# Kernel tuning notes

Hardware: AMD Instinct MI355X
Metric: run time of the kernel (lower is better)

The kernel has to match this reference:

```python
import jax, jax.numpy as jnp
import numpy as np

B, N, Kn, D, L = 4, 2048, 30, 128, 3

def setup_inputs():
    key = jax.random.key(0)
    ks = jax.random.split(key, 16)
    def nrm(k, shape, fan_in):
        return jax.random.normal(k, shape, dtype=jnp.float32) * (1.0 / np.sqrt(fan_in))
    return {
        "V": jax.random.normal(ks[0], (B, N, D), dtype=jnp.float32),
        "E": jax.random.normal(ks[1], (B, N, Kn, D), dtype=jnp.float32),
        "K": jax.random.randint(ks[2], (B, N, Kn), 0, N),
        "Z": jax.random.normal(ks[3], (B, N, D), dtype=jnp.float32),
        "t": jax.random.uniform(ks[4], (B,), dtype=jnp.float32) * 999.0 + 1.0,
        "edge_mask": jnp.ones((B, N, Kn), dtype=bool),
        "sm_W1": nrm(ks[5], (2 * D, D), 2 * D),
        "sm_b1": jnp.zeros((D,), jnp.float32),
        "sm_W2": nrm(ks[6], (D, D), D),
        "sm_b2": jnp.zeros((D,), jnp.float32),
        "sm_ada_W": nrm(ks[7], (D, 2 * D), D),
        "sm_ada_b": jnp.zeros((2 * D,), jnp.float32),
        "msg_W1": nrm(ks[8], (L, 3 * D, D), 3 * D),
        "msg_b1": jnp.zeros((L, D), jnp.float32),
        "msg_W2": nrm(ks[9], (L, D, D), D),
        "msg_b2": jnp.zeros((L, D), jnp.float32),
        "ada1_W": nrm(ks[10], (L, D, 2 * D), D),
        "ada1_b": jnp.zeros((L, 2 * D), jnp.float32),
        "ffn_W1": nrm(ks[11], (L, D, D), D),
        "ffn_b1": jnp.zeros((L, D), jnp.float32),
        "ffn_W2": nrm(ks[12], (L, D, D), D),
        "ffn_b2": jnp.zeros((L, D), jnp.float32),
        "ada2_W": nrm(ks[13], (L, D, 2 * D), D),
        "ada2_b": jnp.zeros((L, 2 * D), jnp.float32),
        "proj_W": nrm(ks[14], (D, D), D),
    }

def _ln(x):
    mu = x.mean(-1, keepdims=True)
    var = ((x - mu) ** 2).mean(-1, keepdims=True)
    return (x - mu) * jax.lax.rsqrt(var + 1e-5)

def _adaln(x, tf, W, b):
    # adaLN: LayerNorm (no affine) modulated by time features -> scale/shift
    g, bt = jnp.split(tf @ W + b, 2, axis=-1)  # each [B,1,D]
    return _ln(x) * (1.0 + g) + bt

def _featurize_t(t):
    wn = 10000.0 ** (-jnp.arange(0, D, 2, dtype=jnp.float32) / D)   # [D/2]
    phase = t[:, None, None] * wn[None, None, :]                    # [B,1,D/2]
    tf = jnp.stack([jnp.sin(phase), jnp.cos(phase)], axis=-1)       # [B,1,D/2,2] interleaved sin/cos
    return tf.reshape(t.shape[0], 1, D)

def reference(V, E, K, Z, t, edge_mask, sm_W1, sm_b1, sm_W2, sm_b2, sm_ada_W, sm_ada_b,
              msg_W1, msg_b1, msg_W2, msg_b2, ada1_W, ada1_b, ffn_W1, ffn_b1,
              ffn_W2, ffn_b2, ada2_W, ada2_b, proj_W):
    tf = _featurize_t(t)                                 # [B,1,D]
    VZ = jnp.concatenate([V, Z], axis=-1)                # [B,N,2D]
    h = jax.nn.gelu(VZ @ sm_W1 + sm_b1) @ sm_W2 + sm_b2  # sequence messenger MLP
    V = _adaln(V + h, tf, sm_ada_W, sm_ada_b)
    bidx = jnp.arange(V.shape[0])[:, None, None]
    for l in range(L):
        Vj = V[bidx, K]                                  # gather neighbors [B,N,Kn,D]
        Vi = jnp.broadcast_to(V[:, :, None, :], Vj.shape)
        Min = jnp.concatenate([Vi, E, Vj], axis=-1)      # [B,N,Kn,3D]
        msg = jax.nn.gelu(Min @ msg_W1[l] + msg_b1[l]) @ msg_W2[l] + msg_b2[l]
        msg = jnp.where(edge_mask[..., None], msg, 0.0)
        dV = msg.sum(axis=2) / Kn                        # aggregate over neighbors
        V = _adaln(V + dV, tf, ada1_W[l], ada1_b[l])
        h = jax.nn.gelu(V @ ffn_W1[l] + ffn_b1[l]) @ ffn_W2[l] + ffn_b2[l]
        V = _adaln(V + h, tf, ada2_W[l], ada2_b[l])
    return V @ proj_W
```

## Files before the change

kernel.cpp:

```cpp
#include <hip/hip_runtime.h>
#include <hip/hip_bf16.h>

#define DEV static __device__ __forceinline__

typedef __bf16 bf16x8 __attribute__((ext_vector_type(8)));
typedef unsigned short u16x8 __attribute__((ext_vector_type(8)));
typedef unsigned short u16x4 __attribute__((ext_vector_type(4)));
typedef float f32x4 __attribute__((ext_vector_type(4)));

#if __has_builtin(__builtin_amdgcn_exp2f)
#define EXP2F(x) __builtin_amdgcn_exp2f(x)
#else
#define EXP2F(x) exp2f(x)
#endif
#if __has_builtin(__builtin_amdgcn_rcpf)
#define RCPF(x) __builtin_amdgcn_rcpf(x)
#else
#define RCPF(x) (1.0f / (x))
#endif


DEV unsigned short f2bfh(float f) {
    return __builtin_bit_cast(unsigned short, (__bf16)f);
}

DEV float bf2f(unsigned short v) {
    return __builtin_bit_cast(float, (unsigned)v << 16);
}

DEV float gelu_f(float x) {
    float x2 = x * x;
    float t  = __builtin_fmaf(-0.10294324f, x2, -2.3022082f);
    float e  = EXP2F(x * t);
    return x * RCPF(1.0f + e);
}

DEV f32x4 mfma16(bf16x8 a, bf16x8 b, f32x4 c) {
    return __builtin_amdgcn_mfma_f32_16x16x32_bf16(a, b, c, 0, 0, 0);
}

DEV bf16x8 cvt8(float4 x, float4 y) {
    bf16x8 r;
    r[0] = (__bf16)x.x; r[1] = (__bf16)x.y; r[2] = (__bf16)x.z; r[3] = (__bf16)x.w;
    r[4] = (__bf16)y.x; r[5] = (__bf16)y.y; r[6] = (__bf16)y.z; r[7] = (__bf16)y.w;
    return r;
}

DEV bf16x8 aload_f32(const float* p) {
    float4 x = *(const float4*)p;
    float4 y = *(const float4*)(p + 4);
    return cvt8(x, y);
}

DEV bf16x8 uload(const unsigned short* p) {
    return __builtin_bit_cast(bf16x8, *(const u16x8*)(p));
}

DEV bf16x8 bload(const unsigned short* WT, int col, int koff) {
    return __builtin_bit_cast(bf16x8, *(const u16x8*)(WT + col * 136 + koff));
}

DEV void stage_wt(unsigned short* WT, const unsigned short* src, int tid, int nthr) {
    for (int i = tid; i < 2048; i += nthr) {
        int n = i >> 4, k0 = (i & 15) << 3;
        *(u16x8*)(WT + n * 136 + k0) = *(const u16x8*)(src + n * 128 + k0);
    }
}

__global__ __launch_bounds__(256) void k_wconv(
    const float* __restrict__ smW1, const float* __restrict__ smW2,
    const float* __restrict__ projW, const float* __restrict__ msgW1,
    const float* __restrict__ msgW2, const float* __restrict__ ffnW1,
    const float* __restrict__ ffnW2, unsigned short* __restrict__ WTG)
{
    int m = blockIdx.x >> 3;
    int chunk = blockIdx.x & 7;
    const float* src;
    if (m == 0) src = smW1;
    else if (m == 1) src = smW1 + 16384;
    else if (m == 2) src = smW2;
    else if (m == 3) src = projW;
    else {
        int mm = m - 4; int l = mm / 6; int j = mm % 6;
        if (j < 3)      src = msgW1 + l * 49152 + j * 16384;
        else if (j == 3) src = msgW2 + l * 16384;
        else if (j == 4) src = ffnW1 + l * 16384;
        else             src = ffnW2 + l * 16384;
    }
    unsigned short* dst = WTG + m * 16384;
    int s0 = chunk * 2048 + threadIdx.x * 8;
    int k = s0 >> 7, n = s0 & 127;
    float4 x = *(const float4*)(src + s0);
    float4 y = *(const float4*)(src + s0 + 4);
    dst[(n + 0) * 128 + k] = f2bfh(x.x);
    dst[(n + 1) * 128 + k] = f2bfh(x.y);
    dst[(n + 2) * 128 + k] = f2bfh(x.z);
    dst[(n + 3) * 128 + k] = f2bfh(x.w);
    dst[(n + 4) * 128 + k] = f2bfh(y.x);
    dst[(n + 5) * 128 + k] = f2bfh(y.y);
    dst[(n + 6) * 128 + k] = f2bfh(y.z);
    dst[(n + 7) * 128 + k] = f2bfh(y.w);
}

__global__ __launch_bounds__(256) void k_prep(
    const float* __restrict__ t,
    const float* __restrict__ smadaW, const float* __restrict__ smadab,
    const float* __restrict__ a1W, const float* __restrict__ a1b,
    const float* __restrict__ a2W, const float* __restrict__ a2b,
    float* __restrict__ MOD)
{
    __shared__ float tf[4][128];
    int tid = threadIdx.x;
    {
        int b = tid >> 6, i = tid & 63;
        float wn = __expf(-(float)i * (9.210340371976184f / 64.0f));
        float ph = t[b] * wn;
        tf[b][2 * i]     = sinf(ph);
        tf[b][2 * i + 1] = cosf(ph);
    }
    __syncthreads();
    int o = blockIdx.x * 256 + tid;
    int b, c;
    const float* W; const float* bias; float* out;
    if (o < 1024) {
        b = o >> 8; c = o & 255; W = smadaW; bias = smadab; out = MOD + o;
    } else if (o < 4096) {
        int oo = o - 1024; int lb = oo >> 8; int l = lb >> 2;
        b = lb & 3; c = oo & 255;
        W = a1W + l * 32768; bias = a1b + l * 256; out = MOD + o;
    } else {
        int oo = o - 4096; int lb = oo >> 8; int l = lb >> 2;
        b = lb & 3; c = oo & 255;
        W = a2W + l * 32768; bias = a2b + l * 256; out = MOD + 4096 + oo;
    }
    float s = bias[c];
    const float* tfb = tf[b];
    #pragma unroll 8
    for (int k = 0; k < 128; ++k) s += tfb[k] * W[k * 256 + c];
    *out = s;
}

__global__ __launch_bounds__(256) void k_msgr(
    const float* __restrict__ V, const float* __restrict__ Z,
    const unsigned short* __restrict__ WTG,
    const float* __restrict__ smb1, const float* __restrict__ smb2,
    const float* __restrict__ MOD, float* __restrict__ Vout)
{
    __shared__ __align__(16) unsigned short WT[128 * 136];
    __shared__ __align__(16) float XB[64 * 132];
    const int tid = threadIdx.x;
    const int w = tid >> 6, l = tid & 63, lr = l & 15, lg = l >> 4;
    const int tok0 = blockIdx.x * 64;
    const int batch = tok0 >> 11;
    const int rowA = tok0 + w * 16 + lr;

    f32x4 acc[8] = {};
    for (int kh = 0; kh < 2; ++kh) {
        __syncthreads();
        stage_wt(WT, WTG + kh * 16384, tid, 256);
        __syncthreads();
        const float* A = (kh == 0) ? V : Z;
        #pragma unroll
        for (int ks = 0; ks < 4; ++ks) {
            bf16x8 a = aload_f32(A + rowA * 128 + ks * 32 + lg * 8);
            #pragma unroll
            for (int c = 0; c < 8; ++c)
                acc[c] = mfma16(a, bload(WT, c * 16 + lr, ks * 32 + lg * 8), acc[c]);
        }
    }
    #pragma unroll
    for (int c = 0; c < 8; ++c) {
        int col = c * 16 + lr;
        float b1v = smb1[col];
        #pragma unroll
        for (int j = 0; j < 4; ++j)
            XB[(w * 16 + lg * 4 + j) * 132 + col] = gelu_f(acc[c][j] + b1v);
    }
    __syncthreads();
    stage_wt(WT, WTG + 2 * 16384, tid, 256);
    __syncthreads();
    f32x4 acc2[8] = {};
    #pragma unroll
    for (int ks = 0; ks < 4; ++ks) {
        bf16x8 a = aload_f32(XB + (w * 16 + lr) * 132 + ks * 32 + lg * 8);
        #pragma unroll
        for (int c = 0; c < 8; ++c)
            acc2[c] = mfma16(a, bload(WT, c * 16 + lr, ks * 32 + lg * 8), acc2[c]);
    }
    const float* MODp = MOD + batch * 256;
    #pragma unroll
    for (int j = 0; j < 4; ++j) {
        int row = tok0 + w * 16 + lg * 4 + j;
        float xv[8], s1 = 0.f, s2 = 0.f;
        #pragma unroll
        for (int c = 0; c < 8; ++c) {
            int col = c * 16 + lr;
            float x = acc2[c][j] + smb2[col] + V[row * 128 + col];
            xv[c] = x; s1 += x; s2 += x * x;
        }
        #pragma unroll
        for (int m = 1; m <= 8; m <<= 1) { s1 += __shfl_xor(s1, m); s2 += __shfl_xor(s2, m); }
        float mu = s1 * (1.0f / 128.0f);
        float var = s2 * (1.0f / 128.0f) - mu * mu;
        float rs = rsqrtf(var + 1e-5f);
        #pragma unroll
        for (int c = 0; c < 8; ++c) {
            int col = c * 16 + lr;
            Vout[row * 128 + col] = (xv[c] - mu) * rs * (1.0f + MODp[col]) + MODp[128 + col];
        }
    }
}

__global__ __launch_bounds__(256) void k_tab(
    const float* __restrict__ Vb, const unsigned short* __restrict__ WTa,
    const unsigned short* __restrict__ WTc, const float* __restrict__ b1,
    float* __restrict__ TAf, unsigned short* __restrict__ TBb)
{
    __shared__ __align__(16) unsigned short WT[128 * 136];
    const int tid = threadIdx.x;
    const int w = tid >> 6, l = tid & 63, lr = l & 15, lg = l >> 4;
    const int tok0 = blockIdx.x * 64;
    const int rowA = tok0 + w * 16 + lr;

    stage_wt(WT, WTa, tid, 256);
    __syncthreads();
    f32x4 acc[8] = {};
    #pragma unroll
    for (int ks = 0; ks < 4; ++ks) {
        bf16x8 a = aload_f32(Vb + rowA * 128 + ks * 32 + lg * 8);
        #pragma unroll
        for (int c = 0; c < 8; ++c)
            acc[c] = mfma16(a, bload(WT, c * 16 + lr, ks * 32 + lg * 8), acc[c]);
    }
    #pragma unroll
    for (int c = 0; c < 8; ++c) {
        int col = c * 16 + lr;
        float b1v = b1[col];
        #pragma unroll
        for (int j = 0; j < 4; ++j) {
            int row = tok0 + w * 16 + lg * 4 + j;
            TAf[row * 128 + col] = acc[c][j] + b1v;
        }
    }
    __syncthreads();
    stage_wt(WT, WTc, tid, 256);
    __syncthreads();
    f32x4 acc2[8] = {};
    #pragma unroll
    for (int ks = 0; ks < 4; ++ks) {
        bf16x8 a = aload_f32(Vb + rowA * 128 + ks * 32 + lg * 8);
        #pragma unroll
        for (int c = 0; c < 8; ++c)
            acc2[c] = mfma16(a, bload(WT, c * 16 + lr, ks * 32 + lg * 8), acc2[c]);
    }
    #pragma unroll
    for (int c = 0; c < 8; ++c) {
        int col = c * 16 + lr;
        #pragma unroll
        for (int j = 0; j < 4; ++j) {
            int row = tok0 + w * 16 + lg * 4 + j;
            TBb[row * 128 + col] = f2bfh(acc2[c][j]);
        }
    }
}

template<int MODE>
__global__ __launch_bounds__(256, 2) void k_edge10(
    const float* __restrict__ E,
    const unsigned short* __restrict__ Ebf,
    unsigned short* __restrict__ EbfW,
    const int* __restrict__ Kidx, const float* __restrict__ TAf,
    const unsigned short* __restrict__ TBb,
    const unsigned short* __restrict__ WTb, float* __restrict__ S)
{
    __shared__ __align__(16) unsigned short ELb[2][32 * 128];
    __shared__ __align__(16) unsigned short TBL[2][32 * 128];
    const int tid = threadIdx.x;
    const int w = tid >> 6, l = tid & 63, lr = l & 15, lg = l >> 4;
    const int nq = w;
    const int t0 = blockIdx.x * 16;
    const int bbase = (t0 >> 11) << 11;

    bf16x8 bfr[8];
    #pragma unroll
    for (int n = 0; n < 2; ++n)
        #pragma unroll
        for (int ks = 0; ks < 4; ++ks)
            bfr[n * 4 + ks] = uload(WTb + (nq * 32 + n * 16 + lr) * 128 + ks * 32 + lg * 8);

    float4 eR[4]; u16x8 eR16[2]; u16x8 tbR[2];
    int ka[2], kb[2], kc[2];

    auto KREAD2 = [&](int tok, int k[2]) {
        #pragma unroll
        for (int it = 0; it < 2; ++it) {
            int r = (it * 256 + tid) >> 4;
            k[it] = (r < 30) ? Kidx[tok * 30 + r] : 0;
        }
    };
    auto EISSUE = [&](int tok) {
        if constexpr (MODE == 2) {
            #pragma unroll
            for (int it = 0; it < 2; ++it)
                eR16[it] = *(const u16x8*)((const char*)Ebf + (size_t)tok * 8192 +
                                           (it * 256 + tid) * 16);
        } else {
            #pragma unroll
            for (int it = 0; it < 4; ++it) {
                int s = it * 256 + tid;
                if (s < 960)
                    eR[it] = *(const float4*)(E + ((size_t)tok * 30 + (s >> 5)) * 128 + (s & 31) * 4);
            }
        }
    };
    auto TBISSUE = [&](const int k[2]) {
        #pragma unroll
        for (int it = 0; it < 2; ++it) {
            int q = (it * 256 + tid) & 15;
            tbR[it] = *(const u16x8*)(TBb + (size_t)(bbase + k[it]) * 128 + q * 8);
        }
    };
    auto SWRITE = [&](int buf, int tok) {
        if constexpr (MODE == 2) {
            #pragma unroll
            for (int it = 0; it < 2; ++it)
                *(u16x8*)((char*)ELb[buf] + (it * 256 + tid) * 16) = eR16[it];
        } else {
            #pragma unroll
            for (int it = 0; it < 4; ++it) {
                int s = it * 256 + tid;
                if (s < 960) {
                    int r = s >> 5, q = s & 31;
                    int soff = r * 256 + ((q * 8) ^ ((r & 7) << 4));
                    u16x4 pk;
                    pk[0] = f2bfh(eR[it].x); pk[1] = f2bfh(eR[it].y);
                    pk[2] = f2bfh(eR[it].z); pk[3] = f2bfh(eR[it].w);
                    *(u16x4*)((char*)ELb[buf] + soff) = pk;
                    if constexpr (MODE == 1)
                        *(u16x4*)((char*)EbfW + (size_t)tok * 8192 + soff) = pk;
                } else if constexpr (MODE == 1) {
                    int r = s >> 5, q = s & 31;
                    int soff = r * 256 + ((q * 8) ^ ((r & 7) << 4));
                    u16x4 z = {0, 0, 0, 0};
                    *(u16x4*)((char*)EbfW + (size_t)tok * 8192 + soff) = z;
                }
            }
        }
        #pragma unroll
        for (int it = 0; it < 2; ++it) {
            int s = it * 256 + tid;
            int r = s >> 4, q = s & 15;
            *(u16x8*)((char*)TBL[buf] + r * 256 + ((q * 16) ^ ((r & 7) << 4))) = tbR[it];
        }
    };

    KREAD2(t0, ka);
    EISSUE(t0);
    TBISSUE(ka);
    KREAD2(t0 + 1, kb);
    SWRITE(0, t0);
    EISSUE(t0 + 1);
    TBISSUE(kb);
    KREAD2(t0 + 2, kc);
    __syncthreads();

    #pragma unroll 1
    for (int i = 0; i < 16; ++i) {
        const int tok = t0 + i;
        const int cur = i & 1;
        float ta[2];
        #pragma unroll
        for (int n = 0; n < 2; ++n) ta[n] = TAf[tok * 128 + nq * 32 + n * 16 + lr];
        float sacc[2] = {0.f, 0.f};
        const char* eb  = (const char*)ELb[cur];
        const char* tbb = (const char*)TBL[cur];
        #pragma unroll
        for (int m = 0; m < 2; ++m) {
            bf16x8 ar[4];
            #pragma unroll
            for (int ks = 0; ks < 4; ++ks)
                ar[ks] = *(const bf16x8*)(eb + (m * 16 + lr) * 256 +
                          (((ks * 32 + lg * 8) * 2) ^ ((lr & 7) << 4)));
            f32x4 acc[2] = {};
            #pragma unroll
            for (int ks = 0; ks < 4; ++ks)
                #pragma unroll
                for (int n = 0; n < 2; ++n)
                    acc[n] = mfma16(ar[ks], bfr[n * 4 + ks], acc[n]);
            #pragma unroll
            for (int n = 0; n < 2; ++n) {
                int c2 = (nq * 32 + n * 16 + lr) * 2;
                #pragma unroll
                for (int j = 0; j < 4; ++j) {
                    int r = m * 16 + lg * 4 + j;
                    if (r < 30) {
                        unsigned short uv = *(const unsigned short*)(tbb + r * 256 + (c2 ^ ((r & 7) << 4)));
                        sacc[n] += gelu_f(acc[n][j] + ta[n] + bf2f(uv));
                    }
                }
            }
        }
        #pragma unroll
        for (int n = 0; n < 2; ++n) {
            sacc[n] += __shfl_xor(sacc[n], 16);
            sacc[n] += __shfl_xor(sacc[n], 32);
        }
        if (l < 16) {
            #pragma unroll
            for (int n = 0; n < 2; ++n)
                S[tok * 128 + nq * 32 + n * 16 + l] = sacc[n];
        }
        if (i < 15) {
            SWRITE(cur ^ 1, t0 + i + 1);
            if (i < 14) {
                EISSUE(t0 + i + 2);
                TBISSUE(kc);
                int tnk = t0 + i + 3; if (tnk > 8191) tnk = 8191;
                KREAD2(tnk, kc);
            }
            __syncthreads();
        }
    }
}

__global__ __launch_bounds__(256) void k_token(
    const float* __restrict__ Sb, const float* __restrict__ Vb,
    const unsigned short* __restrict__ WTW2, const float* __restrict__ b2,
    const unsigned short* __restrict__ WTF1, const float* __restrict__ fb1,
    const unsigned short* __restrict__ WTF2, const float* __restrict__ fb2,
    const unsigned short* __restrict__ WTP,
    const float* __restrict__ MOD1, const float* __restrict__ MOD2,
    float* __restrict__ Vout, int final_)
{
    __shared__ __align__(16) unsigned short WT[128 * 136];
    __shared__ __align__(16) float XB[64 * 132];
    const int tid = threadIdx.x;
    const int w = tid >> 6, l = tid & 63, lr = l & 15, lg = l >> 4;
    const int tok0 = blockIdx.x * 64;
    const int batch = tok0 >> 11;
    const int rloc = w * 16 + lr;

    stage_wt(WT, WTW2, tid, 256);
    __syncthreads();
    f32x4 acc[8] = {};
    #pragma unroll
    for (int ks = 0; ks < 4; ++ks) {
        bf16x8 a = aload_f32(Sb + (tok0 + rloc) * 128 + ks * 32 + lg * 8);
        #pragma unroll
        for (int c = 0; c < 8; ++c)
            acc[c] = mfma16(a, bload(WT, c * 16 + lr, ks * 32 + lg * 8), acc[c]);
    }
    const float* M1 = MOD1 + batch * 256;
    const float* M2 = MOD2 + batch * 256;
    float vp[8][4];
    #pragma unroll
    for (int j = 0; j < 4; ++j) {
        int row = tok0 + w * 16 + lg * 4 + j;
        float xv[8], s1 = 0.f, s2 = 0.f;
        #pragma unroll
        for (int c = 0; c < 8; ++c) {
            int col = c * 16 + lr;
            float x = acc[c][j] * (1.0f / 30.0f) + b2[col] + Vb[row * 128 + col];
            xv[c] = x; s1 += x; s2 += x * x;
        }
        #pragma unroll
        for (int m = 1; m <= 8; m <<= 1) { s1 += __shfl_xor(s1, m); s2 += __shfl_xor(s2, m); }
        float mu = s1 * (1.0f / 128.0f);
        float var = s2 * (1.0f / 128.0f) - mu * mu;
        float rs = rsqrtf(var + 1e-5f);
        #pragma unroll
        for (int c = 0; c < 8; ++c) {
            int col = c * 16 + lr;
            vp[c][j] = (xv[c] - mu) * rs * (1.0f + M1[col]) + M1[128 + col];
        }
    }
    __syncthreads();
    #pragma unroll
    for (int c = 0; c < 8; ++c)
        #pragma unroll
        for (int j = 0; j < 4; ++j)
            XB[(w * 16 + lg * 4 + j) * 132 + c * 16 + lr] = vp[c][j];
    stage_wt(WT, WTF1, tid, 256);
    __syncthreads();
    f32x4 accB[8] = {};
    #pragma unroll
    for (int ks = 0; ks < 4; ++ks) {
        bf16x8 a = aload_f32(XB + rloc * 132 + ks * 32 + lg * 8);
        #pragma unroll
        for (int c = 0; c < 8; ++c)
            accB[c] = mfma16(a, bload(WT, c * 16 + lr, ks * 32 + lg * 8), accB[c]);
    }
    __syncthreads();
    #pragma unroll
    for (int c = 0; c < 8; ++c) {
        int col = c * 16 + lr;
        float bv = fb1[col];
        #pragma unroll
        for (int j = 0; j < 4; ++j)
            XB[(w * 16 + lg * 4 + j) * 132 + col] = gelu_f(accB[c][j] + bv);
    }
    stage_wt(WT, WTF2, tid, 256);
    __syncthreads();
    f32x4 accC[8] = {};
    #pragma unroll
    for (int ks = 0; ks < 4; ++ks) {
        bf16x8 a = aload_f32(XB + rloc * 132 + ks * 32 + lg * 8);
        #pragma unroll
        for (int c = 0; c < 8; ++c)
            accC[c] = mfma16(a, bload(WT, c * 16 + lr, ks * 32 + lg * 8), accC[c]);
    }
    float v2[8][4];
    #pragma unroll
    for (int j = 0; j < 4; ++j) {
        float xv[8], s1 = 0.f, s2 = 0.f;
        #pragma unroll
        for (int c = 0; c < 8; ++c) {
            int col = c * 16 + lr;
            float x = accC[c][j] + fb2[col] + vp[c][j];
            xv[c] = x; s1 += x; s2 += x * x;
        }
        #pragma unroll
        for (int m = 1; m <= 8; m <<= 1) { s1 += __shfl_xor(s1, m); s2 += __shfl_xor(s2, m); }
        float mu = s1 * (1.0f / 128.0f);
        float var = s2 * (1.0f / 128.0f) - mu * mu;
        float rs = rsqrtf(var + 1e-5f);
        #pragma unroll
        for (int c = 0; c < 8; ++c) {
            int col = c * 16 + lr;
            v2[c][j] = (xv[c] - mu) * rs * (1.0f + M2[col]) + M2[128 + col];
        }
    }
    if (!final_) {
        #pragma unroll
        for (int c = 0; c < 8; ++c)
            #pragma unroll
            for (int j = 0; j < 4; ++j)
                Vout[(tok0 + w * 16 + lg * 4 + j) * 128 + c * 16 + lr] = v2[c][j];
    } else {
        __syncthreads();
        #pragma unroll
        for (int c = 0; c < 8; ++c)
            #pragma unroll
            for (int j = 0; j < 4; ++j)
                XB[(w * 16 + lg * 4 + j) * 132 + c * 16 + lr] = v2[c][j];
        stage_wt(WT, WTP, tid, 256);
        __syncthreads();
        f32x4 accD[8] = {};
        #pragma unroll
        for (int ks = 0; ks < 4; ++ks) {
            bf16x8 a = aload_f32(XB + rloc * 132 + ks * 32 + lg * 8);
            #pragma unroll
            for (int c = 0; c < 8; ++c)
                accD[c] = mfma16(a, bload(WT, c * 16 + lr, ks * 32 + lg * 8), accD[c]);
        }
        #pragma unroll
        for (int c = 0; c < 8; ++c)
            #pragma unroll
            for (int j = 0; j < 4; ++j)
                Vout[(tok0 + w * 16 + lg * 4 + j) * 128 + c * 16 + lr] = accD[c][j];
    }
}


extern "C" void kernel_launch(void* const* d_in, const int* in_sizes, int n_in,
                              void* d_out, int out_size, void* d_ws, size_t ws_size,
                              hipStream_t stream)
{
    const float* V     = (const float*)d_in[0];
    const float* E     = (const float*)d_in[1];
    const int*   K     = (const int*)d_in[2];
    const float* Z     = (const float*)d_in[3];
    const float* t     = (const float*)d_in[4];
    const float* smW1   = (const float*)d_in[6];
    const float* smb1   = (const float*)d_in[7];
    const float* smW2   = (const float*)d_in[8];
    const float* smb2   = (const float*)d_in[9];
    const float* smadaW = (const float*)d_in[10];
    const float* smadab = (const float*)d_in[11];
    const float* msgW1  = (const float*)d_in[12];
    const float* msgb1  = (const float*)d_in[13];
    const float* msgW2  = (const float*)d_in[14];
    const float* msgb2  = (const float*)d_in[15];
    const float* a1W    = (const float*)d_in[16];
    const float* a1b    = (const float*)d_in[17];
    const float* fW1    = (const float*)d_in[18];
    const float* fb1    = (const float*)d_in[19];
    const float* fW2    = (const float*)d_in[20];
    const float* fb2    = (const float*)d_in[21];
    const float* a2W    = (const float*)d_in[22];
    const float* a2b    = (const float*)d_in[23];
    const float* projW  = (const float*)d_in[24];

    float* Vbuf = (float*)d_ws;
    float* TAf  = Vbuf + 8192 * 128;
    float* Sb   = TAf + 8192 * 128;
    float* MOD  = Sb + 8192 * 128;
    unsigned short* TBb = (unsigned short*)(MOD + 7168);
    unsigned short* WTG = TBb + 8192 * 128;
    unsigned short* Ebf = WTG + 22 * 16384;

    size_t need = (size_t)(3 * 8192 * 128 + 7168) * 4
                + (size_t)(8192 * 128 + 22 * 16384) * 2
                + (size_t)8192 * 4096 * 2;
    const bool ebf_ok = (ws_size >= need);

    k_wconv<<<dim3(176), dim3(256), 0, stream>>>(smW1, smW2, projW, msgW1, msgW2, fW1, fW2, WTG);
    k_prep<<<dim3(28), dim3(256), 0, stream>>>(t, smadaW, smadab, a1W, a1b, a2W, a2b, MOD);
    k_msgr<<<dim3(128), dim3(256), 0, stream>>>(V, Z, WTG, smb1, smb2, MOD, Vbuf);

    for (int l = 0; l < 3; ++l) {
        const unsigned short* Wl = WTG + (4 + l * 6) * 16384;
        k_tab<<<dim3(128), dim3(256), 0, stream>>>(Vbuf, Wl, Wl + 2 * 16384, msgb1 + l * 128, TAf, TBb);
        if (ebf_ok) {
            if (l == 0)
                k_edge10<1><<<dim3(512), dim3(256), 0, stream>>>(
                    E, Ebf, Ebf, K, TAf, TBb, Wl + 16384, Sb);
            else
                k_edge10<2><<<dim3(512), dim3(256), 0, stream>>>(
                    E, Ebf, Ebf, K, TAf, TBb, Wl + 16384, Sb);
        } else {
            k_edge10<0><<<dim3(512), dim3(256), 0, stream>>>(
                E, Ebf, Ebf, K, TAf, TBb, Wl + 16384, Sb);
        }
        int fin = (l == 2);
        k_token<<<dim3(128), dim3(256), 0, stream>>>(
            Sb, Vbuf, Wl + 3 * 16384, msgb2 + l * 128,
            Wl + 4 * 16384, fb1 + l * 128, Wl + 5 * 16384, fb2 + l * 128,
            WTG + 3 * 16384,
            MOD + 1024 + l * 1024, MOD + 4096 + l * 1024,
            fin ? (float*)d_out : Vbuf, fin);
    }
}
```

Before: 202.4 us.

## Triple-buffer edge kernel and load E/TB tiles directly into LDS

The edge-message kernel moves from double to triple buffering in shared memory and prefetches two tokens ahead. The bf16 E tile and the gathered TB rows are copied with global_load_lds (direct global-to-LDS), which drops the register staging and separate LDS stores; the XOR swizzle is now applied to the global source address. Layer 0 now writes its cached bf16 E copy unswizzled so later layers can swizzle on load. Launch bounds are raised to 3 blocks per SM. The extra buffer increases LDS use, and each load now has to be complete before the barrier, which may limit the occupancy gain.

New measurement: 203.1 us. About the same (+0.3%).

```diff
diff --git a/kernel.cpp b/kernel.cpp
--- a/kernel.cpp
+++ b/kernel.cpp
@@ -65,6 +65,12 @@
         int n = i >> 4, k0 = (i & 15) << 3;
         *(u16x8*)(WT + n * 136 + k0) = *(const u16x8*)(src + n * 128 + k0);
     }
+}
+
+DEV void gload16(const void* g, void* lds) {
+    __builtin_amdgcn_global_load_lds(
+        (const __attribute__((address_space(1))) unsigned*)g,
+        (__attribute__((address_space(3))) unsigned*)lds, 16, 0, 0);
 }
 
 __global__ __launch_bounds__(256) void k_wconv(
@@ -265,7 +271,7 @@
 }
 
 template<int MODE>
-__global__ __launch_bounds__(256, 2) void k_edge10(
+__global__ __launch_bounds__(256, 3) void k_edge11(
     const float* __restrict__ E,
     const unsigned short* __restrict__ Ebf,
     unsigned short* __restrict__ EbfW,
@@ -273,8 +279,8 @@
     const unsigned short* __restrict__ TBb,
     const unsigned short* __restrict__ WTb, float* __restrict__ S)
 {
-    __shared__ __align__(16) unsigned short ELb[2][32 * 128];
-    __shared__ __align__(16) unsigned short TBL[2][32 * 128];
+    __shared__ __align__(16) unsigned short ELb[3][32 * 128];
+    __shared__ __align__(16) unsigned short TBL[3][32 * 128];
     const int tid = threadIdx.x;
     const int w = tid >> 6, l = tid & 63, lr = l & 15, lg = l >> 4;
     const int nq = w;
@@ -288,8 +294,8 @@
         for (int ks = 0; ks < 4; ++ks)
             bfr[n * 4 + ks] = uload(WTb + (nq * 32 + n * 16 + lr) * 128 + ks * 32 + lg * 8);
 
-    float4 eR[4]; u16x8 eR16[2]; u16x8 tbR[2];
-    int ka[2], kb[2], kc[2];
+    float4 eR[4];
+    int kc[2];
 
     auto KREAD2 = [&](int tok, int k[2]) {
         #pragma unroll
@@ -298,76 +304,96 @@
             k[it] = (r < 30) ? Kidx[tok * 30 + r] : 0;
         }
     };
-    auto EISSUE = [&](int tok) {
-        if constexpr (MODE == 2) {
-            #pragma unroll
-            for (int it = 0; it < 2; ++it)
-                eR16[it] = *(const u16x8*)((const char*)Ebf + (size_t)tok * 8192 +
-                                           (it * 256 + tid) * 16);
-        } else {
-            #pragma unroll
-            for (int it = 0; it < 4; ++it) {
-                int s = it * 256 + tid;
-                if (s < 960)
-                    eR[it] = *(const float4*)(E + ((size_t)tok * 30 + (s >> 5)) * 128 + (s & 31) * 4);
-            }
-        }
-    };
-    auto TBISSUE = [&](const int k[2]) {
-        #pragma unroll
-        for (int it = 0; it < 2; ++it) {
-            int q = (it * 256 + tid) & 15;
-            tbR[it] = *(const u16x8*)(TBb + (size_t)(bbase + k[it]) * 128 + q * 8);
-        }
-    };
-    auto SWRITE = [&](int buf, int tok) {
-        if constexpr (MODE == 2) {
-            #pragma unroll
-            for (int it = 0; it < 2; ++it)
-                *(u16x8*)((char*)ELb[buf] + (it * 256 + tid) * 16) = eR16[it];
-        } else {
-            #pragma unroll
-            for (int it = 0; it < 4; ++it) {
-                int s = it * 256 + tid;
-                if (s < 960) {
-                    int r = s >> 5, q = s & 31;
-                    int soff = r * 256 + ((q * 8) ^ ((r & 7) << 4));
-                    u16x4 pk;
-                    pk[0] = f2bfh(eR[it].x); pk[1] = f2bfh(eR[it].y);
-                    pk[2] = f2bfh(eR[it].z); pk[3] = f2bfh(eR[it].w);
-                    *(u16x4*)((char*)ELb[buf] + soff) = pk;
-                    if constexpr (MODE == 1)
-                        *(u16x4*)((char*)EbfW + (size_t)tok * 8192 + soff) = pk;
-                } else if constexpr (MODE == 1) {
-                    int r = s >> 5, q = s & 31;
-                    int soff = r * 256 + ((q * 8) ^ ((r & 7) << 4));
-                    u16x4 z = {0, 0, 0, 0};
-                    *(u16x4*)((char*)EbfW + (size_t)tok * 8192 + soff) = z;
-                }
-            }
-        }
+    auto TBGLOAD = [&](int buf, const int k[2]) {
         #pragma unroll
         for (int it = 0; it < 2; ++it) {
             int s = it * 256 + tid;
             int r = s >> 4, q = s & 15;
-            *(u16x8*)((char*)TBL[buf] + r * 256 + ((q * 16) ^ ((r & 7) << 4))) = tbR[it];
+            const char* src = (const char*)(TBb + (size_t)(bbase + k[it]) * 128)
+                            + (((q ^ (r & 7)) << 4));
+            gload16(src, (char*)TBL[buf] + it * 4096 + (w << 10));
         }
     };
-
-    KREAD2(t0, ka);
-    EISSUE(t0);
-    TBISSUE(ka);
-    KREAD2(t0 + 1, kb);
-    SWRITE(0, t0);
-    EISSUE(t0 + 1);
-    TBISSUE(kb);
-    KREAD2(t0 + 2, kc);
+    auto EGLOAD = [&](int buf, int tok) {
+        #pragma unroll
+        for (int it = 0; it < 2; ++it) {
+            int s = it * 256 + tid;
+            int r = s >> 4, q = s & 15;
+            const char* src = (const char*)Ebf + (size_t)tok * 8192 + r * 256
+                            + (((q ^ (r & 7)) << 4));
+            gload16(src, (char*)ELb[buf] + it * 4096 + (w << 10));
+        }
+    };
+    auto EISSUE = [&](int tok) {
+        #pragma unroll
+        for (int it = 0; it < 4; ++it) {
+            int s = it * 256 + tid;
+            if (s < 960)
+                eR[it] = *(const float4*)(E + ((size_t)tok * 30 + (s >> 5)) * 128 + (s & 31) * 4);
+        }
+    };
+    auto SWRITE_E = [&](int buf, int tok) {
+        #pragma unroll
+        for (int it = 0; it < 4; ++it) {
+            int s = it * 256 + tid;
+            int r = (MODE < 3) ? 0 : 0;
+            if (s < 960) {
+                int rr = s >> 5, q = s & 31;
+                u16x4 pk;
+                pk[0] = f2bfh(eR[it].x); pk[1] = f2bfh(eR[it].y);
+                pk[2] = f2bfh(eR[it].z); pk[3] = f2bfh(eR[it].w);
+                *(u16x4*)((char*)ELb[buf] + rr * 256 + ((q * 8) ^ ((rr & 7) << 4))) = pk;
+                if constexpr (MODE == 1)
+                    *(u16x4*)((char*)EbfW + (size_t)tok * 8192 + rr * 256 + q * 8) = pk;
+            } else if constexpr (MODE == 1) {
+                int rr = s >> 5, q = s & 31;
+                u16x4 z = {0, 0, 0, 0};
+                *(u16x4*)((char*)EbfW + (size_t)tok * 8192 + rr * 256 + q * 8) = z;
+            }
+            (void)r;
+        }
+    };
+
+    if constexpr (MODE == 3) {
+        int ka[2], kb[2];
+        KREAD2(t0, ka);
+        EGLOAD(0, t0);
+        TBGLOAD(0, ka);
+        KREAD2(t0 + 1, kb);
+        EGLOAD(1, t0 + 1);
+        TBGLOAD(1, kb);
+        KREAD2(t0 + 2, kc);
+    } else {
+        int ka[2], kb[2];
+        EISSUE(t0);
+        KREAD2(t0, ka);
+        SWRITE_E(0, t0);
+        TBGLOAD(0, ka);
+        EISSUE(t0 + 1);
+        KREAD2(t0 + 1, kb);
+        SWRITE_E(1, t0 + 1);
+        TBGLOAD(1, kb);
+        EISSUE(t0 + 2);
+        KREAD2(t0 + 2, kc);
+    }
     __syncthreads();
 
     #pragma unroll 1
     for (int i = 0; i < 16; ++i) {
+        if (i + 2 <= 15) {
+            int bufn = (i + 2) % 3;
+            if constexpr (MODE == 3) {
+                EGLOAD(bufn, t0 + i + 2);
+                TBGLOAD(bufn, kc);
+                if (i + 3 <= 15) KREAD2(t0 + i + 3, kc);
+            } else {
+                SWRITE_E(bufn, t0 + i + 2);
+                TBGLOAD(bufn, kc);
+                if (i + 3 <= 15) { EISSUE(t0 + i + 3); KREAD2(t0 + i + 3, kc); }
+            }
+        }
         const int tok = t0 + i;
-        const int cur = i & 1;
+        const int cur = i % 3;
         float ta[2];
         #pragma unroll
         for (int n = 0; n < 2; ++n) ta[n] = TAf[tok * 128 + nq * 32 + n * 16 + lr];
@@ -410,16 +436,7 @@
             for (int n = 0; n < 2; ++n)
                 S[tok * 128 + nq * 32 + n * 16 + l] = sacc[n];
         }
-        if (i < 15) {
-            SWRITE(cur ^ 1, t0 + i + 1);
-            if (i < 14) {
-                EISSUE(t0 + i + 2);
-                TBISSUE(kc);
-                int tnk = t0 + i + 3; if (tnk > 8191) tnk = 8191;
-                KREAD2(tnk, kc);
-            }
-            __syncthreads();
-        }
+        if (i < 15) __syncthreads();
     }
 }
 
@@ -613,13 +630,13 @@
         k_tab<<<dim3(128), dim3(256), 0, stream>>>(Vbuf, Wl, Wl + 2 * 16384, msgb1 + l * 128, TAf, TBb);
         if (ebf_ok) {
             if (l == 0)
-                k_edge10<1><<<dim3(512), dim3(256), 0, stream>>>(
+                k_edge11<1><<<dim3(512), dim3(256), 0, stream>>>(
                     E, Ebf, Ebf, K, TAf, TBb, Wl + 16384, Sb);
             else
-                k_edge10<2><<<dim3(512), dim3(256), 0, stream>>>(
+                k_edge11<3><<<dim3(512), dim3(256), 0, stream>>>(
                     E, Ebf, Ebf, K, TAf, TBb, Wl + 16384, Sb);
         } else {
-            k_edge10<0><<<dim3(512), dim3(256), 0, stream>>>(
+            k_edge11<0><<<dim3(512), dim3(256), 0, stream>>>(
                 E, Ebf, Ebf, K, TAf, TBb, Wl + 16384, Sb);
         }
         int fin = (l == 2);
```
